# Kernel optimization log

Hardware: AMD Instinct MI355X
Metric: run time of the kernel (lower is better)

The kernel has to match this reference:

```python
import jax, jax.numpy as jnp
import numpy as np

EMBED_DIM = 128
NUM_SYMBOLS = 200000
B = 1024
K = 200
PROCESS_STEPS = 4


def setup_inputs() -> dict:
    key = jax.random.key(0)
    ks = jax.random.split(key, 10)
    D = EMBED_DIM
    emb = jax.random.normal(ks[0], (NUM_SYMBOLS + 1, D), jnp.float32) * 0.02
    emb = emb.at[NUM_SYMBOLS].set(0.0)  # padding_idx row
    return {
        "relations": jax.random.randint(ks[1], (B, K), 0, NUM_SYMBOLS),
        "entities": jax.random.randint(ks[2], (B, K), 0, NUM_SYMBOLS),
        "query": jax.random.randint(ks[3], (B,), 0, NUM_SYMBOLS),
        "symbol_emb": emb,
        "gcn_w_w": jax.random.normal(ks[4], (D, 2 * D), jnp.float32) / np.sqrt(2 * D).astype(np.float32),
        "gcn_w_b": jnp.zeros((D,), jnp.float32),
        "p1_w": jax.random.normal(ks[5], (2 * D, D), jnp.float32) / np.sqrt(D).astype(np.float32),
        "p1_b": jnp.zeros((2 * D,), jnp.float32),
        "p2_w": jax.random.normal(ks[6], (D, 2 * D), jnp.float32) / np.sqrt(2 * D).astype(np.float32),
        "p2_b": jnp.zeros((D,), jnp.float32),
        "ln_a": jnp.ones((D,), jnp.float32),
        "ln_b": jnp.zeros((D,), jnp.float32),
        "w_ih": jax.random.normal(ks[7], (8 * D, D), jnp.float32) * 0.05,
        "w_hh": jax.random.normal(ks[8], (8 * D, 2 * D), jnp.float32) * 0.05,
        "b_ih": jnp.zeros((8 * D,), jnp.float32),
        "b_hh": jnp.zeros((8 * D,), jnp.float32),
    }


def _layer_norm(z, a, b, eps=1e-3):
    # repo's LayerNormalization: (z - mu) / (std + eps) * a + b, unbiased std
    mu = jnp.mean(z, axis=-1, keepdims=True)
    sigma = jnp.std(z, axis=-1, ddof=1, keepdims=True)
    return (z - mu) / (sigma + eps) * a + b


def _forward(symbol_emb, gcn_w_w, gcn_w_b, p1_w, p1_b, p2_w, p2_b,
             ln_a, ln_b, w_ih, w_hh, b_ih, b_hh,
             relations, entities, query):
    D = symbol_emb.shape[1]
    # --- neighbor_encoder: gather -> concat -> linear -> neighbor sum -> tanh
    rel_e = symbol_emb[relations]                       # (B, K, D)
    ent_e = symbol_emb[entities]                        # (B, K, D)
    concat = jnp.concatenate([rel_e, ent_e], axis=-1)   # (B, K, 2D)
    out = jnp.einsum('bkf,df->bkd', concat, gcn_w_w) + gcn_w_b
    num_neighbors = jnp.asarray(relations.shape[0], out.dtype)  # code uses relations.size()[0]
    support = jnp.tanh(out.sum(axis=1) / num_neighbors)  # (B, D)
    # --- SupportEncoder: FFN with residual + layernorm (dropout off in eval)
    hidden = jax.nn.relu(support @ p1_w.T + p1_b)        # (B, 2D)
    support_g = _layer_norm(hidden @ p2_w.T + p2_b + support, ln_a, ln_b)
    # --- QueryEncoder: LSTMCell(D, 2D) process block with attention over support
    q = symbol_emb[query]                                # (B, D)
    bsz = q.shape[0]
    h_r = jnp.zeros((bsz, 2 * D), q.dtype)
    c = jnp.zeros((bsz, 2 * D), q.dtype)
    h_out = q
    for _ in range(PROCESS_STEPS):
        gates = q @ w_ih.T + b_ih + h_r @ w_hh.T + b_hh  # (B, 8D)
        i, f, g, o = jnp.split(gates, 4, axis=-1)
        c = jax.nn.sigmoid(f) * c + jax.nn.sigmoid(i) * jnp.tanh(g)
        h_ = jax.nn.sigmoid(o) * jnp.tanh(c)             # (B, 2D)
        h_out = q + h_[:, :D]                            # (B, D)
        attn = jax.nn.softmax(h_out @ support_g.T, axis=1)  # (B, B)
        r = attn @ support_g                             # (B, D)
        h_r = jnp.concatenate([h_out, r], axis=-1)       # (B, 2D)
    query_embeds = h_out
    # --- cosine similarity over dim=1
    cross = jnp.sum(query_embeds * support_g, axis=1)
    n1 = jnp.sum(query_embeds * query_embeds, axis=1)
    n2 = jnp.sum(support_g * support_g, axis=1)
    return cross / jnp.sqrt(n1 * n2)                     # (B,)


def reference(relations, entities, query, symbol_emb, gcn_w_w, gcn_w_b,
              p1_w, p1_b, p2_w, p2_b, ln_a, ln_b, w_ih, w_hh, b_ih, b_hh):
    return _forward(symbol_emb, gcn_w_w, gcn_w_b, p1_w, p1_b, p2_w, p2_b,
                    ln_a, ln_b, w_ih, w_hh, b_ih, b_hh,
                    relations, entities, query)
```

## Files before the change

### kernel.cpp

```cpp
#include <hip/hip_runtime.h>
#include <math.h>

#define D 128
#define B_SZ 1024
#define KNB 200
#define AHW 264
#define QHW 136
#define PW 1048

typedef _Float16 half8 __attribute__((ext_vector_type(8)));
typedef float floatx4 __attribute__((ext_vector_type(4)));

__device__ __forceinline__ float sigmoid_f(float x) { return 1.f / (1.f + __expf(-x)); }
__device__ __forceinline__ float tanh_fast(float x) { return 1.f - 2.f / (__expf(2.f * x) + 1.f); }

__global__ __launch_bounds__(256) void k_cvtw(
    const float* __restrict__ w_ih, const float* __restrict__ w_hh,
    _Float16* __restrict__ w16)
{
    const int i8 = (blockIdx.x * 256 + threadIdx.x) * 8;
    const float* src = (i8 < 131072) ? (w_ih + i8) : (w_hh + (i8 - 131072));
    float4 v0 = *(const float4*)src;
    float4 v1 = *(const float4*)(src + 4);
    half8 h;
    h[0] = (_Float16)v0.x; h[1] = (_Float16)v0.y; h[2] = (_Float16)v0.z; h[3] = (_Float16)v0.w;
    h[4] = (_Float16)v1.x; h[5] = (_Float16)v1.y; h[6] = (_Float16)v1.z; h[7] = (_Float16)v1.w;
    *(half8*)&w16[i8] = h;
}

__global__ __launch_bounds__(512) void k_support(
    const int* __restrict__ relations, const int* __restrict__ entities,
    const int* __restrict__ query, const float* __restrict__ emb,
    const float* __restrict__ gcn_w, const float* __restrict__ gcn_b,
    const float* __restrict__ p1_w, const float* __restrict__ p1_b,
    const float* __restrict__ p2_w, const float* __restrict__ p2_b,
    const float* __restrict__ ln_a, const float* __restrict__ ln_b,
    float* __restrict__ sg, _Float16* __restrict__ sgH, _Float16* __restrict__ sgT,
    float* __restrict__ qb, _Float16* __restrict__ qbH)
{
    __shared__ int idxs[2 * KNB];
    __shared__ __align__(16) float part[16][132];
    __shared__ __align__(16) float S[2 * D];
    __shared__ __align__(16) float sup[D];
    __shared__ __align__(16) float hid[2 * D];
    __shared__ __align__(16) float zv[D];
    __shared__ float red2[2];

    const int b = blockIdx.x;
    const int t = threadIdx.x;

    if (t < KNB) idxs[t] = relations[b * KNB + t];
    else if (t < 2 * KNB) idxs[t] = entities[b * KNB + (t - KNB)];
    __syncthreads();

    {
        const int g = t >> 5, c4 = (t & 31) * 4;
        const int* mi = &idxs[(g >> 3) * KNB];
        float4 a4 = make_float4(0.f, 0.f, 0.f, 0.f);
        #pragma unroll 5
        for (int k = (g & 7); k < KNB; k += 8) {
            float4 v = *(const float4*)&emb[(size_t)mi[k] * D + c4];
            a4.x += v.x; a4.y += v.y; a4.z += v.z; a4.w += v.w;
        }
        *(float4*)&part[g][c4] = a4;
    }
    __syncthreads();
    if (t < 2 * D) {
        const int half = t >> 7, c = t & 127;
        float s = 0.f;
        #pragma unroll
        for (int j = 0; j < 8; ++j) s += part[half * 8 + j][c];
        S[t] = s;
    }
    __syncthreads();

    if (t < D) {
        const float4* w4 = (const float4*)(gcn_w + t * 2 * D);
        float dot = 0.f;
        #pragma unroll 8
        for (int f = 0; f < 2 * D / 4; ++f) {
            float4 w = w4[f];
            float4 s = *(const float4*)&S[f * 4];
            dot += w.x * s.x + w.y * s.y + w.z * s.z + w.w * s.w;
        }
        float v = (dot + 200.f * gcn_b[t]) * (1.f / 1024.f);
        sup[t] = tanhf(v);
    }
    __syncthreads();

    if (t < 2 * D) {
        const float4* w4 = (const float4*)(p1_w + t * D);
        float dot = 0.f;
        #pragma unroll 8
        for (int f = 0; f < D / 4; ++f) {
            float4 w = w4[f];
            float4 s = *(const float4*)&sup[f * 4];
            dot += w.x * s.x + w.y * s.y + w.z * s.z + w.w * s.w;
        }
        float h = dot + p1_b[t];
        hid[t] = h > 0.f ? h : 0.f;
    }
    __syncthreads();

    if (t < D) {
        const float4* w4 = (const float4*)(p2_w + t * 2 * D);
        float dot = 0.f;
        #pragma unroll 8
        for (int f = 0; f < 2 * D / 4; ++f) {
            float4 w = w4[f];
            float4 s = *(const float4*)&hid[f * 4];
            dot += w.x * s.x + w.y * s.y + w.z * s.z + w.w * s.w;
        }
        zv[t] = dot + p2_b[t] + sup[t];
    }
    __syncthreads();

    if (t < 64) {
        float x0 = zv[t], x1 = zv[t + 64];
        float s = x0 + x1;
        for (int off = 32; off; off >>= 1) s += __shfl_down(s, off);
        float mu = __shfl(s, 0) * (1.f / 128.f);
        float d0 = x0 - mu, d1 = x1 - mu;
        float v = d0 * d0 + d1 * d1;
        for (int off = 32; off; off >>= 1) v += __shfl_down(v, off);
        v = __shfl(v, 0);
        if (t == 0) { red2[0] = mu; red2[1] = sqrtf(v * (1.f / 127.f)); }
    }
    __syncthreads();
    if (t < D) {
        float mu = red2[0], sigma = red2[1];
        float val = (zv[t] - mu) / (sigma + 1e-3f) * ln_a[t] + ln_b[t];
        sg[b * D + t] = val;
        sgH[b * D + t] = (_Float16)val;
        sgT[t * B_SZ + b] = (_Float16)val;
        float qv = emb[(size_t)query[b] * D + t];
        qb[b * D + t] = qv;
        qbH[b * D + t] = (_Float16)qv;
    }
}

__global__ __launch_bounds__(1024) void k_lstm(
    const _Float16* __restrict__ qbH, const float* __restrict__ qb,
    const _Float16* __restrict__ sgH, const _Float16* __restrict__ sgT,
    const float* __restrict__ sg, const _Float16* __restrict__ w16,
    const float* __restrict__ b_ih, const float* __restrict__ b_hh,
    float* __restrict__ out)
{
    __shared__ _Float16 Ah[16 * AHW];
    __shared__ _Float16 qH[16 * QHW];
    __shared__ _Float16 P[16 * PW];
    __shared__ float qF[16][132];
    __shared__ float hF[16][132];
    __shared__ float rpar[2][16][132];
    __shared__ float pred[16][17];
    __shared__ float mrow[16];
    __shared__ float sinv[16];

    const int t = threadIdx.x;
    const int w = t >> 6, lane = t & 63;
    const int m = lane & 15, quad = lane >> 4;
    const int b0 = blockIdx.x * 16;
    const int u = w * 16 + m;

    if (t < 256) {
        const int row = t >> 4, c = (t & 15) * 8;
        *(half8*)&qH[row * QHW + c] = *(const half8*)&qbH[(b0 + row) * D + c];
    }
    if (t < 512) {
        const int row = t >> 5, c = (t & 31) * 4;
        *(float4*)&qF[row][c] = *(const float4*)&qb[(b0 + row) * D + c];
    }
    float bi[4];
    #pragma unroll
    for (int g = 0; g < 4; ++g) bi[g] = b_ih[g * 256 + u] + b_hh[g * 256 + u];
    __syncthreads();

    floatx4 gqr[4];
    #pragma unroll
    for (int g = 0; g < 4; ++g)
        #pragma unroll
        for (int z = 0; z < 4; ++z) gqr[g][z] = 0.f;
    #pragma unroll
    for (int ks = 0; ks < 4; ++ks) {
        half8 a = *(const half8*)&qH[m * QHW + ks * 32 + quad * 8];
        #pragma unroll
        for (int g = 0; g < 4; ++g) {
            half8 bf = *(const half8*)&w16[(g * 256 + u) * D + ks * 32 + quad * 8];
            gqr[g] = __builtin_amdgcn_mfma_f32_16x16x32_f16(a, bf, gqr[g], 0, 0, 0);
        }
    }

    float creg[4];
    #pragma unroll
    for (int rr = 0; rr < 4; ++rr) {
        float gi = gqr[0][rr] + bi[0];
        float gg = gqr[2][rr] + bi[2];
        float go = gqr[3][rr] + bi[3];
        float cn = sigmoid_f(gi) * tanh_fast(gg);
        creg[rr] = cn;
        if (w < 8) {
            const int row = quad * 4 + rr;
            float ho = qF[row][u] + sigmoid_f(go) * tanh_fast(cn);
            Ah[row * AHW + u] = (_Float16)ho;
            hF[row][u] = ho;
        }
    }
    __syncthreads();

    #pragma unroll 1
    for (int s = 0; s < 3; ++s) {
        floatx4 a2[4];
        #pragma unroll
        for (int i = 0; i < 4; ++i)
            #pragma unroll
            for (int z = 0; z < 4; ++z) a2[i][z] = 0.f;
        #pragma unroll
        for (int ks = 0; ks < 4; ++ks) {
            half8 a = *(const half8*)&Ah[m * AHW + ks * 32 + quad * 8];
            #pragma unroll
            for (int i = 0; i < 4; ++i) {
                const int j0 = (w * 4 + i) * 16;
                half8 bf = *(const half8*)&sgH[(j0 + m) * D + ks * 32 + quad * 8];
                a2[i] = __builtin_amdgcn_mfma_f32_16x16x32_f16(a, bf, a2[i], 0, 0, 0);
            }
        }

        float mloc[4];
        #pragma unroll
        for (int rr = 0; rr < 4; ++rr) {
            mloc[rr] = fmaxf(fmaxf(a2[0][rr], a2[1][rr]), fmaxf(a2[2][rr], a2[3][rr]));
        }
        #pragma unroll
        for (int off = 1; off <= 8; off <<= 1)
            #pragma unroll
            for (int rr = 0; rr < 4; ++rr)
                mloc[rr] = fmaxf(mloc[rr], __shfl_xor(mloc[rr], off));
        if (m == 0) {
            #pragma unroll
            for (int rr = 0; rr < 4; ++rr) pred[w][quad * 4 + rr] = mloc[rr];
        }
        __syncthreads();
        if (t < 16) {
            float mm = -1e30f;
            #pragma unroll
            for (int ww = 0; ww < 16; ++ww) mm = fmaxf(mm, pred[ww][t]);
            mrow[t] = mm;
        }
        __syncthreads();

        float sloc[4] = {0.f, 0.f, 0.f, 0.f};
        #pragma unroll
        for (int i = 0; i < 4; ++i) {
            const int col = (w * 4 + i) * 16 + m;
            #pragma unroll
            for (int rr = 0; rr < 4; ++rr) {
                const int row = quad * 4 + rr;
                float e = __expf(a2[i][rr] - mrow[row]);
                P[row * PW + col] = (_Float16)e;
                sloc[rr] += e;
            }
        }
        #pragma unroll
        for (int off = 1; off <= 8; off <<= 1)
            #pragma unroll
            for (int rr = 0; rr < 4; ++rr)
                sloc[rr] += __shfl_xor(sloc[rr], off);
        if (m == 0) {
            #pragma unroll
            for (int rr = 0; rr < 4; ++rr) pred[w][quad * 4 + rr] = sloc[rr];
        }
        __syncthreads();
        if (t < 16) {
            float ss = 0.f;
            #pragma unroll
            for (int ww = 0; ww < 16; ++ww) ss += pred[ww][t];
            sinv[t] = 1.f / ss;
        }

        {
            const int nt = w & 7, kh = w >> 3;
            floatx4 a3;
            #pragma unroll
            for (int z = 0; z < 4; ++z) a3[z] = 0.f;
            #pragma unroll
            for (int ks = 0; ks < 16; ++ks) {
                const int kk = kh * 16 + ks;
                half8 a = *(const half8*)&P[m * PW + kk * 32 + quad * 8];
                half8 bf = *(const half8*)&sgT[(nt * 16 + m) * B_SZ + kk * 32 + quad * 8];
                a3 = __builtin_amdgcn_mfma_f32_16x16x32_f16(a, bf, a3, 0, 0, 0);
            }
            #pragma unroll
            for (int rr = 0; rr < 4; ++rr)
                rpar[kh][quad * 4 + rr][nt * 16 + m] = a3[rr];
        }
        __syncthreads();

        #pragma unroll
        for (int half2 = 0; half2 < 2; ++half2) {
            const int e = t + half2 * 1024;
            const int row = e >> 7, dd = e & 127;
            float v = (rpar[0][row][dd] + rpar[1][row][dd]) * sinv[row];
            Ah[row * AHW + 128 + dd] = (_Float16)v;
        }
        __syncthreads();

        floatx4 acc[4];
        #pragma unroll
        for (int g = 0; g < 4; ++g) acc[g] = gqr[g];
        #pragma unroll
        for (int ks = 0; ks < 8; ++ks) {
            half8 a = *(const half8*)&Ah[m * AHW + ks * 32 + quad * 8];
            #pragma unroll
            for (int g = 0; g < 4; ++g) {
                half8 bf = *(const half8*)&w16[131072 + (g * 256 + u) * 256 + ks * 32 + quad * 8];
                acc[g] = __builtin_amdgcn_mfma_f32_16x16x32_f16(a, bf, acc[g], 0, 0, 0);
            }
        }
        __syncthreads();

        #pragma unroll
        for (int rr = 0; rr < 4; ++rr) {
            float gi = acc[0][rr] + bi[0];
            float gf = acc[1][rr] + bi[1];
            float gg = acc[2][rr] + bi[2];
            float go = acc[3][rr] + bi[3];
            float cn = sigmoid_f(gf) * creg[rr] + sigmoid_f(gi) * tanh_fast(gg);
            creg[rr] = cn;
            if (w < 8) {
                const int row = quad * 4 + rr;
                float ho = qF[row][u] + sigmoid_f(go) * tanh_fast(cn);
                Ah[row * AHW + u] = (_Float16)ho;
                hF[row][u] = ho;
            }
        }
        __syncthreads();
    }

    {
        const int row = w;
        float a0 = hF[row][lane], a1 = hF[row][lane + 64];
        float s0 = sg[(b0 + row) * D + lane], s1 = sg[(b0 + row) * D + lane + 64];
        float cr = a0 * s0 + a1 * s1;
        float n1 = a0 * a0 + a1 * a1;
        float n2 = s0 * s0 + s1 * s1;
        for (int off = 32; off; off >>= 1) {
            cr += __shfl_down(cr, off);
            n1 += __shfl_down(n1, off);
            n2 += __shfl_down(n2, off);
        }
        if (lane == 0) out[b0 + row] = cr / sqrtf(n1 * n2);
    }
}

extern "C" void kernel_launch(void* const* d_in, const int* in_sizes, int n_in,
                              void* d_out, int out_size, void* d_ws, size_t ws_size,
                              hipStream_t stream)
{
    const int*   relations = (const int*)d_in[0];
    const int*   entities  = (const int*)d_in[1];
    const int*   query     = (const int*)d_in[2];
    const float* emb       = (const float*)d_in[3];
    const float* gcn_w     = (const float*)d_in[4];
    const float* gcn_b     = (const float*)d_in[5];
    const float* p1_w      = (const float*)d_in[6];
    const float* p1_b      = (const float*)d_in[7];
    const float* p2_w      = (const float*)d_in[8];
    const float* p2_b      = (const float*)d_in[9];
    const float* ln_a      = (const float*)d_in[10];
    const float* ln_b      = (const float*)d_in[11];
    const float* w_ih      = (const float*)d_in[12];
    const float* w_hh      = (const float*)d_in[13];
    const float* b_ih      = (const float*)d_in[14];
    const float* b_hh      = (const float*)d_in[15];

    float* ws = (float*)d_ws;
    float*     sg   = ws;
    float*     qb   = ws + 131072;
    _Float16*  sgH  = (_Float16*)(ws + 262144);
    _Float16*  sgT  = (_Float16*)(ws + 327680);
    _Float16*  qbH  = (_Float16*)(ws + 393216);
    _Float16*  w16  = (_Float16*)(ws + 458752);

    k_cvtw<<<dim3(192), dim3(256), 0, stream>>>(w_ih, w_hh, w16);
    k_support<<<dim3(B_SZ), dim3(512), 0, stream>>>(
        relations, entities, query, emb, gcn_w, gcn_b,
        p1_w, p1_b, p2_w, p2_b, ln_a, ln_b, sg, sgH, sgT, qb, qbH);
    k_lstm<<<dim3(64), dim3(1024), 0, stream>>>(
        qbH, qb, sgH, sgT, sg, w16, b_ih, b_hh, (float*)d_out);
}
```

Baseline: 377.1 us.

## Recompute input-gate projection every LSTM step via a concatenated [q|h|r] operand

The precomputed q@w_ih gate contribution (gqr), which was held in registers, is removed. Each of the four steps now runs one fused K=384 MFMA pass over an Ah buffer laid out as [q | h_out | r], and the first step is handled inside the loop with h and r zeroed. This frees the 16 accumulator registers and the separate qH buffer, which may reduce register pressure. In exchange it adds redundant MFMA work and extra global weight loads for the q part on every step.

```diff
diff --git a/kernel.cpp b/kernel.cpp
--- a/kernel.cpp
+++ b/kernel.cpp
@@ -4,8 +4,7 @@
 #define D 128
 #define B_SZ 1024
 #define KNB 200
-#define AHW 264
-#define QHW 136
+#define AHW 392
 #define PW 1048
 
 typedef _Float16 half8 __attribute__((ext_vector_type(8)));
@@ -147,7 +146,6 @@
     float* __restrict__ out)
 {
     __shared__ _Float16 Ah[16 * AHW];
-    __shared__ _Float16 qH[16 * QHW];
     __shared__ _Float16 P[16 * PW];
     __shared__ float qF[16][132];
     __shared__ float hF[16][132];
@@ -164,155 +162,139 @@
 
     if (t < 256) {
         const int row = t >> 4, c = (t & 15) * 8;
-        *(half8*)&qH[row * QHW + c] = *(const half8*)&qbH[(b0 + row) * D + c];
+        *(half8*)&Ah[row * AHW + c] = *(const half8*)&qbH[(b0 + row) * D + c];
     }
     if (t < 512) {
         const int row = t >> 5, c = (t & 31) * 4;
         *(float4*)&qF[row][c] = *(const float4*)&qb[(b0 + row) * D + c];
     }
+    if (t < 512) {
+        const int row = t >> 5, c = (t & 31) * 8 + 128;
+        half8 z;
+        #pragma unroll
+        for (int i = 0; i < 8; ++i) z[i] = (_Float16)0.f;
+        *(half8*)&Ah[row * AHW + c] = z;
+    }
     float bi[4];
     #pragma unroll
     for (int g = 0; g < 4; ++g) bi[g] = b_ih[g * 256 + u] + b_hh[g * 256 + u];
-    __syncthreads();
-
-    floatx4 gqr[4];
-    #pragma unroll
-    for (int g = 0; g < 4; ++g)
-        #pragma unroll
-        for (int z = 0; z < 4; ++z) gqr[g][z] = 0.f;
-    #pragma unroll
-    for (int ks = 0; ks < 4; ++ks) {
-        half8 a = *(const half8*)&qH[m * QHW + ks * 32 + quad * 8];
-        #pragma unroll
-        for (int g = 0; g < 4; ++g) {
-            half8 bf = *(const half8*)&w16[(g * 256 + u) * D + ks * 32 + quad * 8];
-            gqr[g] = __builtin_amdgcn_mfma_f32_16x16x32_f16(a, bf, gqr[g], 0, 0, 0);
-        }
-    }
-
-    float creg[4];
-    #pragma unroll
-    for (int rr = 0; rr < 4; ++rr) {
-        float gi = gqr[0][rr] + bi[0];
-        float gg = gqr[2][rr] + bi[2];
-        float go = gqr[3][rr] + bi[3];
-        float cn = sigmoid_f(gi) * tanh_fast(gg);
-        creg[rr] = cn;
-        if (w < 8) {
-            const int row = quad * 4 + rr;
-            float ho = qF[row][u] + sigmoid_f(go) * tanh_fast(cn);
-            Ah[row * AHW + u] = (_Float16)ho;
-            hF[row][u] = ho;
-        }
-    }
+    float creg[4] = {0.f, 0.f, 0.f, 0.f};
     __syncthreads();
 
     #pragma unroll 1
-    for (int s = 0; s < 3; ++s) {
-        floatx4 a2[4];
-        #pragma unroll
-        for (int i = 0; i < 4; ++i)
-            #pragma unroll
-            for (int z = 0; z < 4; ++z) a2[i][z] = 0.f;
-        #pragma unroll
-        for (int ks = 0; ks < 4; ++ks) {
+    for (int s = 0; s < 4; ++s) {
+        if (s > 0) {
+            floatx4 a2[4];
+            #pragma unroll
+            for (int i = 0; i < 4; ++i)
+                #pragma unroll
+                for (int z = 0; z < 4; ++z) a2[i][z] = 0.f;
+            #pragma unroll
+            for (int ks = 0; ks < 4; ++ks) {
+                half8 a = *(const half8*)&Ah[m * AHW + 128 + ks * 32 + quad * 8];
+                #pragma unroll
+                for (int i = 0; i < 4; ++i) {
+                    const int j0 = (w * 4 + i) * 16;
+                    half8 bf = *(const half8*)&sgH[(j0 + m) * D + ks * 32 + quad * 8];
+                    a2[i] = __builtin_amdgcn_mfma_f32_16x16x32_f16(a, bf, a2[i], 0, 0, 0);
+                }
+            }
+
+            float mloc[4];
+            #pragma unroll
+            for (int rr = 0; rr < 4; ++rr)
+                mloc[rr] = fmaxf(fmaxf(a2[0][rr], a2[1][rr]), fmaxf(a2[2][rr], a2[3][rr]));
+            #pragma unroll
+            for (int off = 1; off <= 8; off <<= 1)
+                #pragma unroll
+                for (int rr = 0; rr < 4; ++rr)
+                    mloc[rr] = fmaxf(mloc[rr], __shfl_xor(mloc[rr], off));
+            if (m == 0) {
+                #pragma unroll
+                for (int rr = 0; rr < 4; ++rr) pred[w][quad * 4 + rr] = mloc[rr];
+            }
+            __syncthreads();
+            if (t < 16) {
+                float mm = -1e30f;
+                #pragma unroll
+                for (int ww = 0; ww < 16; ++ww) mm = fmaxf(mm, pred[ww][t]);
+                mrow[t] = mm;
+            }
+            __syncthreads();
+
+            float sloc[4] = {0.f, 0.f, 0.f, 0.f};
+            #pragma unroll
+            for (int i = 0; i < 4; ++i) {
+                const int col = (w * 4 + i) * 16 + m;
+                #pragma unroll
+                for (int rr = 0; rr < 4; ++rr) {
+                    const int row = quad * 4 + rr;
+                    float e = __expf(a2[i][rr] - mrow[row]);
+                    P[row * PW + col] = (_Float16)e;
+                    sloc[rr] += e;
+                }
+            }
+            #pragma unroll
+            for (int off = 1; off <= 8; off <<= 1)
+                #pragma unroll
+                for (int rr = 0; rr < 4; ++rr)
+                    sloc[rr] += __shfl_xor(sloc[rr], off);
+            if (m == 0) {
+                #pragma unroll
+                for (int rr = 0; rr < 4; ++rr) pred[w][quad * 4 + rr] = sloc[rr];
+            }
+            __syncthreads();
+            if (t < 16) {
+                float ss = 0.f;
+                #pragma unroll
+                for (int ww = 0; ww < 16; ++ww) ss += pred[ww][t];
+                sinv[t] = 1.f / ss;
+            }
+
+            {
+                const int nt = w & 7, kh = w >> 3;
+                floatx4 a3;
+                #pragma unroll
+                for (int z = 0; z < 4; ++z) a3[z] = 0.f;
+                #pragma unroll
+                for (int ks = 0; ks < 16; ++ks) {
+                    const int kk = kh * 16 + ks;
+                    half8 a = *(const half8*)&P[m * PW + kk * 32 + quad * 8];
+                    half8 bf = *(const half8*)&sgT[(nt * 16 + m) * B_SZ + kk * 32 + quad * 8];
+                    a3 = __builtin_amdgcn_mfma_f32_16x16x32_f16(a, bf, a3, 0, 0, 0);
+                }
+                #pragma unroll
+                for (int rr = 0; rr < 4; ++rr)
+                    rpar[kh][quad * 4 + rr][nt * 16 + m] = a3[rr];
+            }
+            __syncthreads();
+
+            #pragma unroll
+            for (int half2 = 0; half2 < 2; ++half2) {
+                const int e = t + half2 * 1024;
+                const int row = e >> 7, dd = e & 127;
+                float v = (rpar[0][row][dd] + rpar[1][row][dd]) * sinv[row];
+                Ah[row * AHW + 256 + dd] = (_Float16)v;
+            }
+            __syncthreads();
+        }
+
+        floatx4 acc[4];
+        #pragma unroll
+        for (int g = 0; g < 4; ++g)
+            #pragma unroll
+            for (int z = 0; z < 4; ++z) acc[g][z] = 0.f;
+        #pragma unroll
+        for (int ks = 0; ks < 12; ++ks) {
             half8 a = *(const half8*)&Ah[m * AHW + ks * 32 + quad * 8];
             #pragma unroll
-            for (int i = 0; i < 4; ++i) {
-                const int j0 = (w * 4 + i) * 16;
-                half8 bf = *(const half8*)&sgH[(j0 + m) * D + ks * 32 + quad * 8];
-                a2[i] = __builtin_amdgcn_mfma_f32_16x16x32_f16(a, bf, a2[i], 0, 0, 0);
-            }
-        }
-
-        float mloc[4];
-        #pragma unroll
-        for (int rr = 0; rr < 4; ++rr) {
-            mloc[rr] = fmaxf(fmaxf(a2[0][rr], a2[1][rr]), fmaxf(a2[2][rr], a2[3][rr]));
-        }
-        #pragma unroll
-        for (int off = 1; off <= 8; off <<= 1)
-            #pragma unroll
-            for (int rr = 0; rr < 4; ++rr)
-                mloc[rr] = fmaxf(mloc[rr], __shfl_xor(mloc[rr], off));
-        if (m == 0) {
-            #pragma unroll
-            for (int rr = 0; rr < 4; ++rr) pred[w][quad * 4 + rr] = mloc[rr];
-        }
-        __syncthreads();
-        if (t < 16) {
-            float mm = -1e30f;
-            #pragma unroll
-            for (int ww = 0; ww < 16; ++ww) mm = fmaxf(mm, pred[ww][t]);
-            mrow[t] = mm;
-        }
-        __syncthreads();
-
-        float sloc[4] = {0.f, 0.f, 0.f, 0.f};
-        #pragma unroll
-        for (int i = 0; i < 4; ++i) {
-            const int col = (w * 4 + i) * 16 + m;
-            #pragma unroll
-            for (int rr = 0; rr < 4; ++rr) {
-                const int row = quad * 4 + rr;
-                float e = __expf(a2[i][rr] - mrow[row]);
-                P[row * PW + col] = (_Float16)e;
-                sloc[rr] += e;
-            }
-        }
-        #pragma unroll
-        for (int off = 1; off <= 8; off <<= 1)
-            #pragma unroll
-            for (int rr = 0; rr < 4; ++rr)
-                sloc[rr] += __shfl_xor(sloc[rr], off);
-        if (m == 0) {
-            #pragma unroll
-            for (int rr = 0; rr < 4; ++rr) pred[w][quad * 4 + rr] = sloc[rr];
-        }
-        __syncthreads();
-        if (t < 16) {
-            float ss = 0.f;
-            #pragma unroll
-            for (int ww = 0; ww < 16; ++ww) ss += pred[ww][t];
-            sinv[t] = 1.f / ss;
-        }
-
-        {
-            const int nt = w & 7, kh = w >> 3;
-            floatx4 a3;
-            #pragma unroll
-            for (int z = 0; z < 4; ++z) a3[z] = 0.f;
-            #pragma unroll
-            for (int ks = 0; ks < 16; ++ks) {
-                const int kk = kh * 16 + ks;
-                half8 a = *(const half8*)&P[m * PW + kk * 32 + quad * 8];
-                half8 bf = *(const half8*)&sgT[(nt * 16 + m) * B_SZ + kk * 32 + quad * 8];
-                a3 = __builtin_amdgcn_mfma_f32_16x16x32_f16(a, bf, a3, 0, 0, 0);
-            }
-            #pragma unroll
-            for (int rr = 0; rr < 4; ++rr)
-                rpar[kh][quad * 4 + rr][nt * 16 + m] = a3[rr];
-        }
-        __syncthreads();
-
-        #pragma unroll
-        for (int half2 = 0; half2 < 2; ++half2) {
-            const int e = t + half2 * 1024;
-            const int row = e >> 7, dd = e & 127;
-            float v = (rpar[0][row][dd] + rpar[1][row][dd]) * sinv[row];
-            Ah[row * AHW + 128 + dd] = (_Float16)v;
-        }
-        __syncthreads();
-
-        floatx4 acc[4];
-        #pragma unroll
-        for (int g = 0; g < 4; ++g) acc[g] = gqr[g];
-        #pragma unroll
-        for (int ks = 0; ks < 8; ++ks) {
-            half8 a = *(const half8*)&Ah[m * AHW + ks * 32 + quad * 8];
-            #pragma unroll
             for (int g = 0; g < 4; ++g) {
-                half8 bf = *(const half8*)&w16[131072 + (g * 256 + u) * 256 + ks * 32 + quad * 8];
+                const int row = g * 256 + u;
+                half8 bf;
+                if (ks < 4)
+                    bf = *(const half8*)&w16[(size_t)row * 128 + ks * 32 + quad * 8];
+                else
+                    bf = *(const half8*)&w16[131072 + (size_t)row * 256 + (ks - 4) * 32 + quad * 8];
                 acc[g] = __builtin_amdgcn_mfma_f32_16x16x32_f16(a, bf, acc[g], 0, 0, 0);
             }
         }
@@ -329,7 +311,7 @@
             if (w < 8) {
                 const int row = quad * 4 + rr;
                 float ho = qF[row][u] + sigmoid_f(go) * tanh_fast(cn);
-                Ah[row * AHW + u] = (_Float16)ho;
+                Ah[row * AHW + 128 + u] = (_Float16)ho;
                 hF[row][u] = ho;
             }
         }
```

Measured after the change: 389.8 us. +3.4%, slower.
